# Kernel optimization log

Measured on AMD Instinct MI355X. Metric: run time of the kernel, lower is better.

Reference implementation:

```python
import jax, jax.numpy as jnp
import numpy as np

B, N, D, H = 4, 2048, 256, 4
DH = D // H  # 64
TWO_PI = 6.283185307179586


def rotate_half(x):
    # pairs (x0,x1)->(-x1,x0), matching torch unflatten/unbind/stack/flatten
    x1 = x[..., 0::2]
    x2 = x[..., 1::2]
    return jnp.stack((-x2, x1), axis=-1).reshape(x.shape)


def _heads(x):  # [B,N,D] -> [B,H,N,DH]
    return x.reshape(x.shape[0], x.shape[1], H, DH).transpose(0, 2, 1, 3)


def _merge(x):  # [B,H,N,DH] -> [B,N,D]
    return x.transpose(0, 2, 1, 3).reshape(x.shape[0], x.shape[2], H * DH)


def _ffn(x, msg, W1, b1, g, beta, W2, b2):
    h = jnp.concatenate([x, msg], axis=-1) @ W1 + b1
    mu = jnp.mean(h, axis=-1, keepdims=True)
    var = jnp.mean((h - mu) ** 2, axis=-1, keepdims=True)
    h = (h - mu) * jax.lax.rsqrt(var + 1e-5) * g + beta
    h = jax.nn.gelu(h, approximate=False)  # torch nn.GELU() is erf-based
    return x + h @ W2 + b2


def _self_block(d, kp, Wqkv, bqkv, Wo, bo, W1, b1, g, beta, W2, b2):
    b, n = d.shape[0], d.shape[1]
    # torch: unflatten(-1,(H,-1,3)) -> per-head last dim arranged [DH,3]
    qkv = (d @ Wqkv + bqkv).reshape(b, n, H, DH, 3).transpose(0, 2, 1, 3, 4)
    q, k, v = qkv[..., 0], qkv[..., 1], qkv[..., 2]
    q = q * kp[0] + rotate_half(q) * kp[1]
    k = k * kp[0] + rotate_half(k) * kp[1]
    sim = jnp.einsum('bhid,bhjd->bhij', q, k) * (DH ** -0.5)
    a = jax.nn.softmax(sim, axis=-1)
    ctx = _merge(jnp.einsum('bhij,bhjd->bhid', a, v))
    msg = ctx @ Wo + bo
    return _ffn(d, msg, W1, b1, g, beta, W2, b2)


def _sdpa(q, k, v):
    a = jax.nn.softmax(jnp.einsum('bhid,bhjd->bhij', q, k) * (DH ** -0.5), axis=-1)
    return jnp.einsum('bhij,bhjd->bhid', a, v)


def _cross_block(d0, d1, Wqk, bqk, Wv, bv, Wo, bo, W1, b1, g, beta, W2, b2):
    qk0 = _heads(d0 @ Wqk + bqk)
    qk1 = _heads(d1 @ Wqk + bqk)
    v0 = _heads(d0 @ Wv + bv)
    v1 = _heads(d1 @ Wv + bv)
    m0 = _merge(_sdpa(qk0, qk1, v1)) @ Wo + bo
    m1 = _merge(_sdpa(qk1, qk0, v0)) @ Wo + bo
    return _ffn(d0, m0, W1, b1, g, beta, W2, b2), _ffn(d1, m1, W1, b1, g, beta, W2, b2)


def setup_inputs() -> dict:
    key = jax.random.key(0)
    ks = jax.random.split(key, 32)
    def w(k, shape, fan_in):
        return jax.random.normal(k, shape, jnp.float32) / np.sqrt(fan_in)
    ang0 = jax.random.uniform(ks[0], (B, 1, N, DH), jnp.float32) * TWO_PI
    ang1 = jax.random.uniform(ks[1], (B, 1, N, DH), jnp.float32) * TWO_PI
    inp = {
        'keypoints0': jnp.stack([jnp.cos(ang0), jnp.sin(ang0)]),
        'keypoints1': jnp.stack([jnp.cos(ang1), jnp.sin(ang1)]),
        'descriptors0': jax.random.normal(ks[2], (B, N, D), jnp.float32),
        'descriptors1': jax.random.normal(ks[3], (B, N, D), jnp.float32),
        'sa_Wqkv': w(ks[4], (D, 3 * D), D), 'sa_bqkv': w(ks[5], (3 * D,), D),
        'sa_Wo': w(ks[6], (D, D), D), 'sa_bo': w(ks[7], (D,), D),
        'sa_W1': w(ks[8], (2 * D, 2 * D), 2 * D), 'sa_b1': w(ks[9], (2 * D,), 2 * D),
        'sa_g': jnp.ones((2 * D,), jnp.float32), 'sa_beta': jnp.zeros((2 * D,), jnp.float32),
        'sa_W2': w(ks[10], (2 * D, D), 2 * D), 'sa_b2': w(ks[11], (D,), 2 * D),
        'ca_Wqk': w(ks[12], (D, D), D), 'ca_bqk': w(ks[13], (D,), D),
        'ca_Wv': w(ks[14], (D, D), D), 'ca_bv': w(ks[15], (D,), D),
        'ca_Wo': w(ks[16], (D, D), D), 'ca_bo': w(ks[17], (D,), D),
        'ca_W1': w(ks[18], (2 * D, 2 * D), 2 * D), 'ca_b1': w(ks[19], (2 * D,), 2 * D),
        'ca_g': jnp.ones((2 * D,), jnp.float32), 'ca_beta': jnp.zeros((2 * D,), jnp.float32),
        'ca_W2': w(ks[20], (2 * D, D), 2 * D), 'ca_b2': w(ks[21], (D,), 2 * D),
    }
    return inp


def reference(keypoints0, keypoints1, descriptors0, descriptors1,
              sa_Wqkv, sa_bqkv, sa_Wo, sa_bo, sa_W1, sa_b1, sa_g, sa_beta, sa_W2, sa_b2,
              ca_Wqk, ca_bqk, ca_Wv, ca_bv, ca_Wo, ca_bo, ca_W1, ca_b1, ca_g, ca_beta, ca_W2, ca_b2):
    d0 = _self_block(descriptors0, keypoints0, sa_Wqkv, sa_bqkv, sa_Wo, sa_bo,
                     sa_W1, sa_b1, sa_g, sa_beta, sa_W2, sa_b2)
    d1 = _self_block(descriptors1, keypoints1, sa_Wqkv, sa_bqkv, sa_Wo, sa_bo,
                     sa_W1, sa_b1, sa_g, sa_beta, sa_W2, sa_b2)
    return _cross_block(d0, d1, ca_Wqk, ca_bqk, ca_Wv, ca_bv, ca_Wo, ca_bo,
                        ca_W1, ca_b1, ca_g, ca_beta, ca_W2, ca_b2)
```

## Files before the change

### kernel.cpp

```cpp
#include <hip/hip_runtime.h>
#include <hip/hip_bf16.h>

typedef unsigned short u16;
typedef short bf16x8 __attribute__((ext_vector_type(8)));
typedef unsigned short u16x8 __attribute__((ext_vector_type(8)));
typedef float f32x4 __attribute__((ext_vector_type(4)));
typedef float f32x16 __attribute__((ext_vector_type(16)));

#define NB 4
#define NS 2048
#define DM 256
#define NH 4
#define DHD 64
#define MR (NB*NS)
#define BHC (NB*NH)
#define BH2 32
#define M2 (2*MR)
#define ACH 4
#define ACK (NS/ACH)
#define HS ((size_t)BHC*NS*DHD)

__device__ __forceinline__ u16 f2b(float f){
    __hip_bfloat16 h = __float2bfloat16(f);
    return __builtin_bit_cast(u16, h);
}
__device__ __forceinline__ float b2f(u16 u){
    unsigned v = ((unsigned)u) << 16; float f; __builtin_memcpy(&f, &v, 4); return f;
}
__device__ __forceinline__ float fexp2(float x){
    float r; asm("v_exp_f32 %0, %1" : "=v"(r) : "v"(x)); return r;
}

#define MFMA16(a,b,c) __builtin_amdgcn_mfma_f32_16x16x32_bf16((a),(b),(c),0,0,0)
#define MFMA32(a,b,c) __builtin_amdgcn_mfma_f32_32x32x16_bf16((a),(b),(c),0,0,0)

__global__ void k_cast_desc(const float* __restrict__ d0, const float* __restrict__ d1, u16* __restrict__ dst){
    int i = (blockIdx.x*256 + threadIdx.x)*4;
    if (i + 3 >= 2*MR*DM) return;
    const float* src = (i < MR*DM) ? d0 : d1;
    int j = (i < MR*DM) ? i : i - MR*DM;
    float4 v = *(const float4*)(src + j);
    dst[i+0] = f2b(v.x); dst[i+1] = f2b(v.y); dst[i+2] = f2b(v.z); dst[i+3] = f2b(v.w);
}
__device__ __forceinline__ void wt_one(const float* W, u16* Wt, int idx, int K, int Nc){
    int k = idx % K, nc = idx / K;
    Wt[idx] = f2b(W[(size_t)k*Nc + nc]);
}
__global__ void k_cwt1(const float* __restrict__ W, u16* __restrict__ Wt, int K, int Nc){
    int idx = blockIdx.x*256 + threadIdx.x;
    if (idx < K*Nc) wt_one(W, Wt, idx, K, Nc);
}
__global__ void k_cwt4(const float* W0, const float* W1, const float* W2, const float* W3,
                       u16* T0, u16* T1, u16* T2, u16* T3){
    int idx = blockIdx.x*256 + threadIdx.x;
    int w = idx >> 16, j = idx & 65535;
    const float* W = (w==0)?W0:(w==1)?W1:(w==2)?W2:W3;
    u16* T = (w==0)?T0:(w==1)?T1:(w==2)?T2:T3;
    wt_one(W, T, j, 256, 256);
}
__global__ void k_cwt2a(const float* W0, const float* W1, u16* T0, u16* T1){
    int idx = blockIdx.x*256 + threadIdx.x;
    int w = idx >> 18, j = idx & 262143;
    wt_one(w? W1:W0, w? T1:T0, j, 512, 512);
}
__global__ void k_cwt2b(const float* W0, const float* W1, u16* T0, u16* T1){
    int idx = blockIdx.x*256 + threadIdx.x;
    int w = idx >> 17, j = idx & 131071;
    wt_one(w? W1:W0, w? T1:T0, j, 512, 256);
}
__global__ void k_fill_x(const u16* __restrict__ Xb, u16* __restrict__ cat){
    int i = blockIdx.x*256 + threadIdx.x;
    if (i >= M2*DM/8) return;
    int row = i >> 5, c8 = i & 31;
    *(u16x8*)(cat + (size_t)row*512 + c8*8) = *(const u16x8*)(Xb + (size_t)row*256 + c8*8);
}

#define GEMM_CORE(Aptr, Wptr, Kdim) \
    __shared__ __attribute__((aligned(16))) u16 As[64*72]; \
    __shared__ __attribute__((aligned(16))) u16 Bs[64*72]; \
    const int tid = threadIdx.x; \
    const int lane = tid & 63, widx = tid >> 6; \
    const int wr = widx >> 1, wc = widx & 1; \
    const int r16 = lane & 15, g = lane >> 4; \
    const int m0 = blockIdx.x * 64, n0 = blockIdx.y * 64; \
    f32x4 acc[2][2] = {}; \
    { const int nkt = (Kdim) >> 6; \
    for (int kt = 0; kt < nkt; ++kt){ \
        _Pragma("unroll") \
        for (int it = 0; it < 2; ++it){ \
            int ch = tid + it*256; \
            int row = ch >> 3, cc = ch & 7; \
            *(u16x8*)(As + row*72 + cc*8) = *(const u16x8*)((Aptr) + (size_t)(m0+row)*(Kdim) + kt*64 + cc*8); \
            *(u16x8*)(Bs + row*72 + cc*8) = *(const u16x8*)((Wptr) + (size_t)(n0+row)*(Kdim) + kt*64 + cc*8); \
        } \
        __syncthreads(); \
        _Pragma("unroll") \
        for (int s = 0; s < 2; ++s){ \
            bf16x8 a0 = *(const bf16x8*)(As + (wr*32 +      r16)*72 + s*32 + g*8); \
            bf16x8 a1 = *(const bf16x8*)(As + (wr*32 + 16 + r16)*72 + s*32 + g*8); \
            bf16x8 b0 = *(const bf16x8*)(Bs + (wc*32 +      r16)*72 + s*32 + g*8); \
            bf16x8 b1 = *(const bf16x8*)(Bs + (wc*32 + 16 + r16)*72 + s*32 + g*8); \
            acc[0][0] = MFMA16(a0, b0, acc[0][0]); \
            acc[0][1] = MFMA16(a0, b1, acc[0][1]); \
            acc[1][0] = MFMA16(a1, b0, acc[1][0]); \
            acc[1][1] = MFMA16(a1, b1, acc[1][1]); \
        } \
        __syncthreads(); \
    } }

__global__ __launch_bounds__(256) void k_gemm(const u16* __restrict__ A, const u16* __restrict__ Wt,
                                              const float* __restrict__ bias, float* __restrict__ C,
                                              int K, int Nc){
    GEMM_CORE(A, Wt, K)
#pragma unroll
    for (int mi = 0; mi < 2; ++mi)
#pragma unroll
    for (int ni = 0; ni < 2; ++ni){
        int row = m0 + wr*32 + mi*16 + g*4;
        int col = n0 + wc*32 + ni*16 + r16;
        float bc = bias[col];
        float* cp = C + (size_t)row*Nc + col;
#pragma unroll
        for (int rr = 0; rr < 4; ++rr) cp[(size_t)rr*Nc] = acc[mi][ni][rr] + bc;
    }
}
__global__ __launch_bounds__(256) void k_gemm_cat(const u16* __restrict__ A, const u16* __restrict__ Wt,
                                                  const float* __restrict__ bias, u16* __restrict__ cat,
                                                  int K){
    GEMM_CORE(A, Wt, K)
#pragma unroll
    for (int mi = 0; mi < 2; ++mi)
#pragma unroll
    for (int ni = 0; ni < 2; ++ni){
        int row = m0 + wr*32 + mi*16 + g*4;
        int col = n0 + wc*32 + ni*16 + r16;
        float bc = bias[col];
        u16* cp = cat + (size_t)row*512 + 256 + col;
#pragma unroll
        for (int rr = 0; rr < 4; ++rr) cp[(size_t)rr*512] = f2b(acc[mi][ni][rr] + bc);
    }
}
__global__ __launch_bounds__(256) void k_gemm_qk(const u16* __restrict__ A, const u16* __restrict__ Wt,
                                                 const float* __restrict__ bias,
                                                 u16* __restrict__ dstQ, u16* __restrict__ dstK, int K){
    GEMM_CORE(A, Wt, K)
#pragma unroll
    for (int mi = 0; mi < 2; ++mi)
#pragma unroll
    for (int ni = 0; ni < 2; ++ni){
        int row = m0 + wr*32 + mi*16 + g*4;
        int col = n0 + wc*32 + ni*16 + r16;
        float bc = bias[col];
        int h = col >> 6, dh = col & 63;
#pragma unroll
        for (int rr = 0; rr < 4; ++rr){
            int r2 = row + rr;
            int b = r2 >> 11, n = r2 & (NS-1);
            u16 v = f2b(acc[mi][ni][rr] + bc);
            size_t off = ((size_t)(b*NH + h)*NS + n)*DHD + dh;
            dstQ[off] = v;
            dstK[off] = v;
        }
    }
}
__global__ __launch_bounds__(256) void k_gemm_vt(const u16* __restrict__ A, const u16* __restrict__ Wt,
                                                 const float* __restrict__ bias, u16* __restrict__ VT, int K){
    GEMM_CORE(A, Wt, K)
#pragma unroll
    for (int mi = 0; mi < 2; ++mi)
#pragma unroll
    for (int ni = 0; ni < 2; ++ni){
        int row = m0 + wr*32 + mi*16 + g*4;
        int col = n0 + wc*32 + ni*16 + r16;
        float bc = bias[col];
        int h = col >> 6, dh = col & 63;
#pragma unroll
        for (int rr = 0; rr < 4; ++rr){
            int r2 = row + rr;
            int b = r2 >> 11, n = r2 & (NS-1);
            VT[((size_t)(b*NH + h)*DHD + dh)*NS + n] = f2b(acc[mi][ni][rr] + bc);
        }
    }
}
__global__ __launch_bounds__(256) void k_gemm_resid_mid(const u16* __restrict__ A, const u16* __restrict__ Wt,
                                                        const float* __restrict__ bias,
                                                        const float* __restrict__ X0, const float* __restrict__ X1,
                                                        u16* __restrict__ OutB, int K){
    GEMM_CORE(A, Wt, K)
#pragma unroll
    for (int mi = 0; mi < 2; ++mi)
#pragma unroll
    for (int ni = 0; ni < 2; ++ni){
        int row = m0 + wr*32 + mi*16 + g*4;
        int col = n0 + wc*32 + ni*16 + r16;
        float bc = bias[col];
#pragma unroll
        for (int rr = 0; rr < 4; ++rr){
            int r2 = row + rr;
            const float* X = (r2 < MR) ? X0 : X1;
            size_t xi = (size_t)(r2 < MR ? r2 : r2 - MR)*DM + col;
            OutB[(size_t)r2*DM + col] = f2b(acc[mi][ni][rr] + bc + X[xi]);
        }
    }
}
__global__ __launch_bounds__(256) void k_gemm_resid_out(const u16* __restrict__ A, const u16* __restrict__ Wt,
                                                        const float* __restrict__ bias,
                                                        const u16* __restrict__ Xb, float* __restrict__ OutF, int K){
    GEMM_CORE(A, Wt, K)
#pragma unroll
    for (int mi = 0; mi < 2; ++mi)
#pragma unroll
    for (int ni = 0; ni < 2; ++ni){
        int row = m0 + wr*32 + mi*16 + g*4;
        int col = n0 + wc*32 + ni*16 + r16;
        float bc = bias[col];
#pragma unroll
        for (int rr = 0; rr < 4; ++rr){
            size_t idx = (size_t)(row+rr)*DM + col;
            OutF[idx] = acc[mi][ni][rr] + bc + b2f(Xb[idx]);
        }
    }
}

__global__ void k_qkv_epi(const float* __restrict__ C, const float* __restrict__ kp,
                          u16* __restrict__ Q, u16* __restrict__ K, u16* __restrict__ VT){
    int idx = blockIdx.x*blockDim.x + threadIdx.x;
    if (idx >= BHC*NS*32) return;
    int dhp = idx & 31;
    int n   = (idx >> 5) & (NS-1);
    int bh  = idx >> 16;
    int b = bh >> 2, h = bh & 3;
    size_t crow = (size_t)(b*NS + n)*768 + h*192 + dhp*6;
    float q0 = C[crow+0], k0 = C[crow+1], v0 = C[crow+2];
    float q1 = C[crow+3], k1 = C[crow+4], v1 = C[crow+5];
    size_t kb = (size_t)b*(NS*DHD) + (size_t)n*DHD + dhp*2;
    float c0 = kp[kb], c1 = kp[kb+1];
    float s0 = kp[kb + (size_t)NB*NS*DHD], s1 = kp[kb + (size_t)NB*NS*DHD + 1];
    float qr0 = q0*c0 - q1*s0, qr1 = q1*c1 + q0*s1;
    float kr0 = k0*c0 - k1*s0, kr1 = k1*c1 + k0*s1;
    size_t qk = ((size_t)bh*NS + n)*DHD + dhp*2;
    Q[qk]   = f2b(qr0); Q[qk+1] = f2b(qr1);
    K[qk]   = f2b(kr0); K[qk+1] = f2b(kr1);
    size_t vt = ((size_t)bh*DHD + dhp*2)*NS + n;
    VT[vt]      = f2b(v0);
    VT[vt + NS] = f2b(v1);
}

__global__ __launch_bounds__(256) void k_attn3(const u16* __restrict__ Q, const u16* __restrict__ Kb,
                                               const u16* __restrict__ VT,
                                               u16* __restrict__ opart, float* __restrict__ mpart,
                                               float* __restrict__ lpart, float scale_l2e){
    const int tid = threadIdx.x, lane = tid & 63, widx = tid >> 6;
    const int l31 = lane & 31, hi = lane >> 5;
    const int gw = blockIdx.x*4 + widx;
    const int bh = gw >> 6, qt = gw & 63;
    const int q0 = qt * 32;
    const int ck = blockIdx.y;

    bf16x8 qf[4];
    {
        const u16* Qp = Q + ((size_t)bh*NS + q0 + l31)*DHD + hi*8;
#pragma unroll
        for (int kk = 0; kk < 4; ++kk){
            u16x8 raw = *(const u16x8*)(Qp + kk*16);
            u16x8 sc;
#pragma unroll
            for (int i = 0; i < 8; ++i) sc[i] = f2b(b2f(raw[i]) * scale_l2e);
            qf[kk] = __builtin_bit_cast(bf16x8, sc);
        }
    }

    f32x16 o0 = {}, o1 = {};
    float m_run = -1e30f, l_run = 0.f;
    const u16* Kbase = Kb + ((size_t)bh*NS + ck*ACK)*DHD;
    const u16* Vb0 = VT + ((size_t)bh*DHD +      l31)*NS + ck*ACK;
    const u16* Vb1 = VT + ((size_t)bh*DHD + 32 + l31)*NS + ck*ACK;

    for (int jt = 0; jt < ACK/32; ++jt){
        const u16* Kp = Kbase + (size_t)(jt*32 + l31)*DHD + hi*8;
        f32x16 s = {};
#pragma unroll
        for (int kk = 0; kk < 4; ++kk){
            bf16x8 kf = *(const bf16x8*)(Kp + kk*16);
            s = MFMA32(kf, qf[kk], s);
        }
        float t[8];
#pragma unroll
        for (int i = 0; i < 8; ++i) t[i] = fmaxf(s[2*i], s[2*i+1]);
#pragma unroll
        for (int i = 0; i < 4; ++i) t[i] = fmaxf(t[i], t[i+4]);
        t[0] = fmaxf(t[0], t[2]); t[1] = fmaxf(t[1], t[3]);
        float mx = fmaxf(t[0], t[1]);
        mx = fmaxf(mx, __shfl_xor(mx, 32));
        if (__any(mx > m_run + 8.0f)){
            float mn = fmaxf(m_run, mx);
            float corr = fexp2(m_run - mn);
            l_run *= corr;
            o0 *= corr; o1 *= corr;
            m_run = mn;
        }
        float p[16];
#pragma unroll
        for (int i = 0; i < 16; ++i) p[i] = fexp2(s[i] - m_run);
        float u[8];
#pragma unroll
        for (int i = 0; i < 8; ++i) u[i] = p[2*i] + p[2*i+1];
#pragma unroll
        for (int i = 0; i < 4; ++i) u[i] = u[i] + u[i+4];
        u[0] += u[2]; u[1] += u[3];
        float sum = u[0] + u[1];
        sum += __shfl_xor(sum, 32);
        l_run += sum;
        unsigned c[8], x[8];
#pragma unroll
        for (int i = 0; i < 8; ++i)
            c[i] = ((unsigned)f2b(p[2*i+1]) << 16) | (unsigned)f2b(p[2*i]);
#pragma unroll
        for (int i = 0; i < 8; ++i) x[i] = __shfl_xor(c[i], 32);
        unsigned pb0w[4], pb1w[4];
        pb0w[0] = hi ? x[2] : c[0];  pb0w[1] = hi ? x[3] : c[1];
        pb0w[2] = hi ? c[2] : x[0];  pb0w[3] = hi ? c[3] : x[1];
        pb1w[0] = hi ? x[6] : c[4];  pb1w[1] = hi ? x[7] : c[5];
        pb1w[2] = hi ? c[6] : x[4];  pb1w[3] = hi ? c[7] : x[5];
        bf16x8 pb0, pb1;
        __builtin_memcpy(&pb0, pb0w, 16);
        __builtin_memcpy(&pb1, pb1w, 16);
        bf16x8 v00 = *(const bf16x8*)(Vb0 + jt*32 +      hi*8);
        bf16x8 v01 = *(const bf16x8*)(Vb0 + jt*32 + 16 + hi*8);
        bf16x8 v10 = *(const bf16x8*)(Vb1 + jt*32 +      hi*8);
        bf16x8 v11 = *(const bf16x8*)(Vb1 + jt*32 + 16 + hi*8);
        o0 = MFMA32(v00, pb0, o0);
        o0 = MFMA32(v01, pb1, o0);
        o1 = MFMA32(v10, pb0, o1);
        o1 = MFMA32(v11, pb1, o1);
    }
    const size_t rq = ((size_t)ck*BH2 + bh)*NS + q0 + l31;
    if (!hi){ mpart[rq] = m_run; lpart[rq] = l_run; }
    u16* op = opart + rq*64;
#pragma unroll
    for (int r = 0; r < 16; ++r){
        int d = (r & 3) + 8*(r >> 2) + 4*hi;
        op[d]      = f2b(o0[r]);
        op[d + 32] = f2b(o1[r]);
    }
}

__global__ __launch_bounds__(256) void k_attn_comb(const u16* __restrict__ opart,
                                                   const float* __restrict__ mpart,
                                                   const float* __restrict__ lpart,
                                                   u16* __restrict__ ctx){
    int idx = blockIdx.x*256 + threadIdx.x;
    if (idx >= BH2*NS*64) return;
    int d = idx & 63; int n = (idx >> 6) & (NS-1); int bh2 = idx >> 17;
    size_t row = (size_t)bh2*NS + n;
    const size_t CH = (size_t)BH2*NS;
    float M = -1e30f;
#pragma unroll
    for (int ck = 0; ck < ACH; ++ck) M = fmaxf(M, mpart[ck*CH + row]);
    float l = 0.f, o = 0.f;
#pragma unroll
    for (int ck = 0; ck < ACH; ++ck){
        float e = fexp2(mpart[ck*CH + row] - M);
        l += lpart[ck*CH + row] * e;
        o += b2f(opart[(ck*CH + row)*64 + d]) * e;
    }
    int side = bh2 >> 4, bh = bh2 & 15;
    int b = bh >> 2, h = bh & 3;
    ctx[((size_t)side*MR + (size_t)b*NS + n)*DM + h*DHD + d] = f2b(o / l);
}

__global__ __launch_bounds__(256) void k_ln_gelu(const float* __restrict__ C, const float* __restrict__ gam,
                                                 const float* __restrict__ bet, u16* __restrict__ hb){
    int row = blockIdx.x, t = threadIdx.x;
    const float* cr = C + (size_t)row*512;
    float x0 = cr[t], x1 = cr[t+256];
    float s = x0 + x1, q = x0*x0 + x1*x1;
#pragma unroll
    for (int offs = 1; offs < 64; offs <<= 1){
        s += __shfl_xor(s, offs);
        q += __shfl_xor(q, offs);
    }
    __shared__ float ss[4], qq[4];
    int w = t >> 6, ln = t & 63;
    if (ln == 0){ ss[w] = s; qq[w] = q; }
    __syncthreads();
    s = ss[0]+ss[1]+ss[2]+ss[3];
    q = qq[0]+qq[1]+qq[2]+qq[3];
    float mu = s * (1.f/512.f);
    float var = q * (1.f/512.f) - mu*mu;
    float rs = rsqrtf(var + 1e-5f);
    float y0 = (x0 - mu)*rs*gam[t]     + bet[t];
    float y1 = (x1 - mu)*rs*gam[t+256] + bet[t+256];
    float g0 = 0.5f*y0*(1.f + erff(y0*0.70710678118654752f));
    float g1 = 0.5f*y1*(1.f + erff(y1*0.70710678118654752f));
    hb[(size_t)row*512 + t]       = f2b(g0);
    hb[(size_t)row*512 + 256 + t] = f2b(g1);
}

extern "C" void kernel_launch(void* const* d_in, const int* in_sizes, int n_in,
                              void* d_out, int out_size, void* d_ws, size_t ws_size,
                              hipStream_t stream)
{
    const float* kp0   = (const float*)d_in[0];
    const float* kp1   = (const float*)d_in[1];
    const float* desc0 = (const float*)d_in[2];
    const float* desc1 = (const float*)d_in[3];
    const float* saWqkv= (const float*)d_in[4];
    const float* sabqkv= (const float*)d_in[5];
    const float* saWo  = (const float*)d_in[6];
    const float* sabo  = (const float*)d_in[7];
    const float* saW1  = (const float*)d_in[8];
    const float* sab1  = (const float*)d_in[9];
    const float* sag   = (const float*)d_in[10];
    const float* sabe  = (const float*)d_in[11];
    const float* saW2  = (const float*)d_in[12];
    const float* sab2  = (const float*)d_in[13];
    const float* caWqk = (const float*)d_in[14];
    const float* cabqk = (const float*)d_in[15];
    const float* caWv  = (const float*)d_in[16];
    const float* cabv  = (const float*)d_in[17];
    const float* caWo  = (const float*)d_in[18];
    const float* cabo  = (const float*)d_in[19];
    const float* caW1  = (const float*)d_in[20];
    const float* cab1  = (const float*)d_in[21];
    const float* cag   = (const float*)d_in[22];
    const float* cabe  = (const float*)d_in[23];
    const float* caW2  = (const float*)d_in[24];
    const float* cab2  = (const float*)d_in[25];

    char* ws = (char*)d_ws;
    size_t off = 0;
    auto alloc = [&](size_t b)->char*{ char* p = ws + off; off = (off + b + 255) & ~(size_t)255; return p; };

    u16* wqkvT = (u16*)alloc(768*256*2);
    u16* woST  = (u16*)alloc(256*256*2);
    u16* w1ST  = (u16*)alloc(512*512*2);
    u16* w2ST  = (u16*)alloc(256*512*2);
    u16* wqkT  = (u16*)alloc(256*256*2);
    u16* wvT   = (u16*)alloc(256*256*2);
    u16* woCT  = (u16*)alloc(256*256*2);
    u16* w1CT  = (u16*)alloc(512*512*2);
    u16* w2CT  = (u16*)alloc(256*512*2);
    u16* X01b  = (u16*)alloc((size_t)M2*DM*2);
    u16* Q2    = (u16*)alloc((size_t)BH2*NS*DHD*2);
    u16* K2    = (u16*)alloc((size_t)BH2*NS*DHD*2);
    u16* V2    = (u16*)alloc((size_t)BH2*NS*DHD*2);
    u16* ctx2  = (u16*)alloc((size_t)M2*DM*2);
    u16* midb2 = (u16*)alloc((size_t)M2*DM*2);
    u16* cat2  = (u16*)alloc((size_t)M2*512*2);
    u16* hb2   = cat2;
    char* uni  = alloc(33554432);
    float* Cbuf = (float*)uni;
    u16*  opart = (u16*)uni;
    float* mpart = (float*)alloc((size_t)ACH*BH2*NS*4);
    float* lpart = (float*)alloc((size_t)ACH*BH2*NS*4);

    k_cwt1 <<<768, 256, 0, stream>>>(saWqkv, wqkvT, 256, 768);
    k_cwt4 <<<1024,256, 0, stream>>>(saWo, caWqk, caWv, caWo, woST, wqkT, wvT, woCT);
    k_cwt2a<<<2048,256, 0, stream>>>(saW1, caW1, w1ST, w1CT);
    k_cwt2b<<<1024,256, 0, stream>>>(saW2, caW2, w2ST, w2CT);
    k_cast_desc<<<4096,256,0,stream>>>(desc0, desc1, X01b);

    const dim3 AG(512, ACH);
    const float SC = 0.125f * 1.44269504088896f;

    k_gemm<<<dim3(128,12),256,0,stream>>>(X01b,            wqkvT, sabqkv, Cbuf, 256, 768);
    k_qkv_epi<<<4096,256,0,stream>>>(Cbuf, kp0, Q2, K2, V2);
    k_gemm<<<dim3(128,12),256,0,stream>>>(X01b + (size_t)MR*DM, wqkvT, sabqkv, Cbuf, 256, 768);
    k_qkv_epi<<<4096,256,0,stream>>>(Cbuf, kp1, Q2 + HS, K2 + HS, V2 + HS);
    k_attn3<<<AG,256,0,stream>>>(Q2, K2, V2, opart, mpart, lpart, SC);
    k_attn_comb<<<16384,256,0,stream>>>(opart, mpart, lpart, ctx2);
    k_fill_x<<<2048,256,0,stream>>>(X01b, cat2);
    k_gemm_cat<<<dim3(256,4),256,0,stream>>>(ctx2, woST, sabo, cat2, 256);
    k_gemm<<<dim3(256,8),256,0,stream>>>(cat2, w1ST, sab1, Cbuf, 512, 512);
    k_ln_gelu<<<16384,256,0,stream>>>(Cbuf, sag, sabe, hb2);
    k_gemm_resid_mid<<<dim3(256,4),256,0,stream>>>(hb2, w2ST, sab2, desc0, desc1, midb2, 512);

    k_gemm_qk<<<dim3(128,4),256,0,stream>>>(midb2,                wqkT, cabqk, Q2,      K2 + HS, 256);
    k_gemm_qk<<<dim3(128,4),256,0,stream>>>(midb2 + (size_t)MR*DM, wqkT, cabqk, Q2 + HS, K2,      256);
    k_gemm_vt<<<dim3(128,4),256,0,stream>>>(midb2 + (size_t)MR*DM, wvT,  cabv,  V2,      256);
    k_gemm_vt<<<dim3(128,4),256,0,stream>>>(midb2,                wvT,  cabv,  V2 + HS, 256);

    k_attn3<<<AG,256,0,stream>>>(Q2, K2, V2, opart, mpart, lpart, SC);
    k_attn_comb<<<16384,256,0,stream>>>(opart, mpart, lpart, ctx2);
    k_fill_x<<<2048,256,0,stream>>>(midb2, cat2);
    k_gemm_cat<<<dim3(256,4),256,0,stream>>>(ctx2, woCT, cabo, cat2, 256);
    k_gemm<<<dim3(256,8),256,0,stream>>>(cat2, w1CT, cab1, Cbuf, 512, 512);
    k_ln_gelu<<<16384,256,0,stream>>>(Cbuf, cag, cabe, hb2);
    k_gemm_resid_out<<<dim3(256,4),256,0,stream>>>(hb2, w2CT, cab2, midb2, (float*)d_out, 512);

    (void)in_sizes; (void)n_in; (void)out_size; (void)ws_size;
}
```

Before: 505.4 us.

## Tune attention kernel: permlane swap, packed bf16 converts, setprio, block swizzle

Rewrites the P-matrix repacking in the attention kernel to use packed bf16 conversion plus v_permlane32_swap instead of eight cross-lane shuffles and selects. It also raises wave priority around the MFMA groups, interleaves the PV MFMAs across the two accumulators, remaps block indices so that consecutive blocks land on different heads/query tiles, and writes the output as packed 32-bit stores. The aim is to cut VALU and cross-lane overhead in the softmax-to-PV path and improve MFMA issue. The swizzle changes the cache access pattern, and the permlane swap depends on the lane layout matching the old shuffle logic.

New measurement: 525.0 us. +3.9%, slower.

```diff
diff --git a/kernel.cpp b/kernel.cpp
--- a/kernel.cpp
+++ b/kernel.cpp
@@ -29,6 +29,12 @@
 }
 __device__ __forceinline__ float fexp2(float x){
     float r; asm("v_exp_f32 %0, %1" : "=v"(r) : "v"(x)); return r;
+}
+__device__ __forceinline__ unsigned cvt_pk(float lo, float hi){
+    unsigned r; asm("v_cvt_pk_bf16_f32 %0, %1, %2" : "=v"(r) : "v"(lo), "v"(hi)); return r;
+}
+__device__ __forceinline__ void pl32swap(unsigned &a, unsigned &b){
+    asm("v_permlane32_swap_b32 %0, %1" : "+v"(a), "+v"(b));
 }
 
 #define MFMA16(a,b,c) __builtin_amdgcn_mfma_f32_16x16x32_bf16((a),(b),(c),0,0,0)
@@ -157,9 +163,9 @@
             int r2 = row + rr;
             int b = r2 >> 11, n = r2 & (NS-1);
             u16 v = f2b(acc[mi][ni][rr] + bc);
-            size_t off = ((size_t)(b*NH + h)*NS + n)*DHD + dh;
-            dstQ[off] = v;
-            dstK[off] = v;
+            size_t off2 = ((size_t)(b*NH + h)*NS + n)*DHD + dh;
+            dstQ[off2] = v;
+            dstK[off2] = v;
         }
     }
 }
@@ -252,7 +258,9 @@
                                                float* __restrict__ lpart, float scale_l2e){
     const int tid = threadIdx.x, lane = tid & 63, widx = tid >> 6;
     const int l31 = lane & 31, hi = lane >> 5;
-    const int gw = blockIdx.x*4 + widx;
+    const int nb = blockIdx.x;
+    const int lb = (nb & 7)*64 + (nb >> 3);
+    const int gw = lb*4 + widx;
     const int bh = gw >> 6, qt = gw & 63;
     const int q0 = qt * 32;
     const int ck = blockIdx.y;
@@ -279,11 +287,13 @@
     for (int jt = 0; jt < ACK/32; ++jt){
         const u16* Kp = Kbase + (size_t)(jt*32 + l31)*DHD + hi*8;
         f32x16 s = {};
+        __builtin_amdgcn_s_setprio(1);
 #pragma unroll
         for (int kk = 0; kk < 4; ++kk){
             bf16x8 kf = *(const bf16x8*)(Kp + kk*16);
             s = MFMA32(kf, qf[kk], s);
         }
+        __builtin_amdgcn_s_setprio(0);
         float t[8];
 #pragma unroll
         for (int i = 0; i < 8; ++i) t[i] = fmaxf(s[2*i], s[2*i+1]);
@@ -311,37 +321,33 @@
         float sum = u[0] + u[1];
         sum += __shfl_xor(sum, 32);
         l_run += sum;
-        unsigned c[8], x[8];
-#pragma unroll
-        for (int i = 0; i < 8; ++i)
-            c[i] = ((unsigned)f2b(p[2*i+1]) << 16) | (unsigned)f2b(p[2*i]);
-#pragma unroll
-        for (int i = 0; i < 8; ++i) x[i] = __shfl_xor(c[i], 32);
-        unsigned pb0w[4], pb1w[4];
-        pb0w[0] = hi ? x[2] : c[0];  pb0w[1] = hi ? x[3] : c[1];
-        pb0w[2] = hi ? c[2] : x[0];  pb0w[3] = hi ? c[3] : x[1];
-        pb1w[0] = hi ? x[6] : c[4];  pb1w[1] = hi ? x[7] : c[5];
-        pb1w[2] = hi ? c[6] : x[4];  pb1w[3] = hi ? c[7] : x[5];
+        unsigned c[8];
+#pragma unroll
+        for (int i = 0; i < 8; ++i) c[i] = cvt_pk(p[2*i], p[2*i+1]);
+        pl32swap(c[0], c[2]); pl32swap(c[1], c[3]);
+        pl32swap(c[4], c[6]); pl32swap(c[5], c[7]);
         bf16x8 pb0, pb1;
-        __builtin_memcpy(&pb0, pb0w, 16);
-        __builtin_memcpy(&pb1, pb1w, 16);
+        { unsigned w[4] = {c[0], c[1], c[2], c[3]}; __builtin_memcpy(&pb0, w, 16); }
+        { unsigned w[4] = {c[4], c[5], c[6], c[7]}; __builtin_memcpy(&pb1, w, 16); }
         bf16x8 v00 = *(const bf16x8*)(Vb0 + jt*32 +      hi*8);
         bf16x8 v01 = *(const bf16x8*)(Vb0 + jt*32 + 16 + hi*8);
         bf16x8 v10 = *(const bf16x8*)(Vb1 + jt*32 +      hi*8);
         bf16x8 v11 = *(const bf16x8*)(Vb1 + jt*32 + 16 + hi*8);
+        __builtin_amdgcn_s_setprio(1);
         o0 = MFMA32(v00, pb0, o0);
+        o1 = MFMA32(v10, pb0, o1);
         o0 = MFMA32(v01, pb1, o0);
-        o1 = MFMA32(v10, pb0, o1);
         o1 = MFMA32(v11, pb1, o1);
+        __builtin_amdgcn_s_setprio(0);
     }
     const size_t rq = ((size_t)ck*BH2 + bh)*NS + q0 + l31;
     if (!hi){ mpart[rq] = m_run; lpart[rq] = l_run; }
-    u16* op = opart + rq*64;
-#pragma unroll
-    for (int r = 0; r < 16; ++r){
+    unsigned* op32 = (unsigned*)(opart + rq*64);
+#pragma unroll
+    for (int r = 0; r < 16; r += 2){
         int d = (r & 3) + 8*(r >> 2) + 4*hi;
-        op[d]      = f2b(o0[r]);
-        op[d + 32] = f2b(o1[r]);
+        op32[d >> 1]        = cvt_pk(o0[r], o0[r+1]);
+        op32[(d >> 1) + 16] = cvt_pk(o1[r], o1[r+1]);
     }
 }
 
@@ -476,10 +482,10 @@
     k_ln_gelu<<<16384,256,0,stream>>>(Cbuf, sag, sabe, hb2);
     k_gemm_resid_mid<<<dim3(256,4),256,0,stream>>>(hb2, w2ST, sab2, desc0, desc1, midb2, 512);
 
-    k_gemm_qk<<<dim3(128,4),256,0,stream>>>(midb2,                wqkT, cabqk, Q2,      K2 + HS, 256);
+    k_gemm_qk<<<dim3(128,4),256,0,stream>>>(midb2,                 wqkT, cabqk, Q2,      K2 + HS, 256);
     k_gemm_qk<<<dim3(128,4),256,0,stream>>>(midb2 + (size_t)MR*DM, wqkT, cabqk, Q2 + HS, K2,      256);
     k_gemm_vt<<<dim3(128,4),256,0,stream>>>(midb2 + (size_t)MR*DM, wvT,  cabv,  V2,      256);
-    k_gemm_vt<<<dim3(128,4),256,0,stream>>>(midb2,                wvT,  cabv,  V2 + HS, 256);
+    k_gemm_vt<<<dim3(128,4),256,0,stream>>>(midb2,                 wvT,  cabv,  V2 + HS, 256);
 
     k_attn3<<<AG,256,0,stream>>>(Q2, K2, V2, opart, mpart, lpart, SC);
     k_attn_comb<<<16384,256,0,stream>>>(opart, mpart, lpart, ctx2);
```
